# Performance work log

Measured on AMD Instinct MI355X. Metric: run time of the kernel, lower is better.

Reference implementation:

```python
import jax, jax.numpy as jnp
import numpy as np

N = 50000      # nodes per side
E = 800000     # edges per side
G = 1024       # graphs per batch
VOCAB = 100000
EMB, GH, EH, OUT = 128, 256, 256, 128
HID = GH + EH


def setup_inputs() -> dict:
    key = jax.random.key(0)
    ks = jax.random.split(key, 32)

    def xav(k, shape):
        lim = float(np.sqrt(6.0 / (shape[0] + shape[1])))
        return jax.random.uniform(k, shape, jnp.float32, -lim, lim)

    inp = {
        "x1": jax.random.randint(ks[0], (N,), 0, 11),
        "edge_index1": jax.random.randint(ks[1], (2, E), 0, N),
        "ent1": jax.random.randint(ks[2], (G,), 0, VOCAB),
        "batch1": jnp.sort(jax.random.randint(ks[3], (N,), 0, G)),
        "x2": jax.random.randint(ks[4], (N,), 0, 11),
        "edge_index2": jax.random.randint(ks[5], (2, E), 0, N),
        "ent2": jax.random.randint(ks[6], (G,), 0, VOCAB),
        "batch2": jnp.sort(jax.random.randint(ks[7], (N,), 0, G)),
        # shared GCN params (xavier weights, zero biases as in _reset_params)
        "atom_emb": xav(ks[8], (11, EMB)),
        "gW1": xav(ks[9], (EMB, GH)), "gb1": jnp.zeros((GH,), jnp.float32),
        "gW2": xav(ks[10], (GH, GH)), "gb2": jnp.zeros((GH,), jnp.float32),
        "fcW": xav(ks[11], (GH, GH)), "fcb": jnp.zeros((GH,), jnp.float32),
        # shared entity encoder params
        "ent_emb": xav(ks[12], (VOCAB, EMB)),
        "eW1": xav(ks[13], (EMB, EH)), "eb1": jnp.zeros((EH,), jnp.float32),
        "eW2": xav(ks[14], (EH, EH)), "eb2": jnp.zeros((EH,), jnp.float32),
        # decoder params
        "dW1": xav(ks[15], (HID, HID)), "db1": jnp.zeros((HID,), jnp.float32),
        "dW2": xav(ks[16], (HID, HID)), "db2": jnp.zeros((HID,), jnp.float32),
        "dW3": xav(ks[17], (HID, OUT)), "db3": jnp.zeros((OUT,), jnp.float32),
    }
    return inp


def _gcn_conv(x, W, b, src, dst, n):
    # PyG GCNConv: self-loops + symmetric normalization, out[dst] += norm * (x@W)[src]
    h = x @ W                                   # [n, d_out]
    loop = jnp.arange(n)
    s = jnp.concatenate([src, loop])
    d = jnp.concatenate([dst, loop])
    deg = jax.ops.segment_sum(jnp.ones_like(s, h.dtype), d, num_segments=n)
    dinv = jnp.where(deg > 0, jax.lax.rsqrt(jnp.maximum(deg, 1e-12)), 0.0)
    norm = dinv[s] * dinv[d]                    # [E+n]
    out = jax.ops.segment_sum(h[s] * norm[:, None], d, num_segments=n)
    return out + b


def _gcn_branch(x, edge_index, batch, atom_emb, gW1, gb1, gW2, gb2, fcW, fcb):
    src, dst = edge_index[0], edge_index[1]
    h = atom_emb[x]                             # [N, EMB]
    h = jax.nn.relu(_gcn_conv(h, gW1, gb1, src, dst, N))
    h = jax.nn.relu(_gcn_conv(h, gW2, gb2, src, dst, N))
    # global mean pool per graph
    counts = jax.ops.segment_sum(jnp.ones((N,), h.dtype), batch, num_segments=G)
    pooled = jax.ops.segment_sum(h, batch, num_segments=G) / jnp.maximum(counts, 1.0)[:, None]
    return pooled @ fcW + fcb                   # [G, GH]


def _enc(ent, ent_emb, eW1, eb1, eW2, eb2):
    e = jax.nn.relu(ent_emb[ent])
    e = jax.nn.relu(e @ eW1 + eb1)
    return jax.nn.relu(e @ eW2 + eb2)           # [G, EH]


def reference(x1, edge_index1, ent1, batch1, x2, edge_index2, ent2, batch2,
              atom_emb, gW1, gb1, gW2, gb2, fcW, fcb,
              ent_emb, eW1, eb1, eW2, eb2,
              dW1, db1, dW2, db2, dW3, db3):
    g1 = _gcn_branch(x1, edge_index1, batch1, atom_emb, gW1, gb1, gW2, gb2, fcW, fcb)
    g2 = _gcn_branch(x2, edge_index2, batch2, atom_emb, gW1, gb1, gW2, gb2, fcW, fcb)
    e1 = _enc(ent1, ent_emb, eW1, eb1, eW2, eb2)
    e2 = _enc(ent2, ent_emb, eW1, eb1, eW2, eb2)
    eg1 = jnp.concatenate([g1, e1], axis=1)     # [G, GH+EH]
    eg2 = jnp.concatenate([g2, e2], axis=1)
    egs = jax.nn.relu(eg1 + eg2)
    h = jax.nn.relu(egs @ dW1 + db1)
    h = jax.nn.relu(h @ dW2 + db2)
    return h @ dW3 + db3                        # [G, OUT]
```

## Files before the change

kernel.cpp:

```cpp
#include <hip/hip_runtime.h>
#include <hip/hip_fp16.h>

static constexpr int kN = 50000;
static constexpr int kE = 800000;
static constexpr int kG = 1024;
static constexpr int kEMB = 128;
static constexpr int kGH = 256;
static constexpr int kEH = 256;
static constexpr int kOUT = 128;
static constexpr int kHID = 512;
static constexpr int kNB = (kN + 255) / 256;
static constexpr int kMD = 64;
static constexpr int kNBKT = 196;
static constexpr int kEPB = 3125;
static constexpr int kPBLK = 256;

typedef __attribute__((ext_vector_type(8))) _Float16 half8v;
typedef __attribute__((ext_vector_type(4))) _Float16 half4v;
typedef __attribute__((ext_vector_type(4))) float floatx4;
typedef __attribute__((ext_vector_type(2))) float floatx2;


#define HS_SCALE 128.0f
#define HS_INV   (1.0f / 128.0f)

__device__ inline void acc_fp8x4(unsigned int w, float& a0, float& a1, float& a2, float& a3) {
    floatx2 lo = __builtin_amdgcn_cvt_pk_f32_fp8(w, false);
    floatx2 hi = __builtin_amdgcn_cvt_pk_f32_fp8(w, true);
    a0 += lo[0]; a1 += lo[1]; a2 += hi[0]; a3 += hi[1];
}

__device__ inline float grp16_reduce(float v) {
    int x;
    x = __builtin_amdgcn_update_dpp(0, __float_as_int(v), 0x121, 0xF, 0xF, true);
    v += __int_as_float(x);
    x = __builtin_amdgcn_update_dpp(0, __float_as_int(v), 0x122, 0xF, 0xF, true);
    v += __int_as_float(x);
    x = __builtin_amdgcn_update_dpp(0, __float_as_int(v), 0x124, 0xF, 0xF, true);
    v += __int_as_float(x);
    x = __builtin_amdgcn_update_dpp(0, __float_as_int(v), 0x128, 0xF, 0xF, true);
    v += __int_as_float(x);
    return v;
}

__global__ void prep_kernel(const float* __restrict__ atom_emb, const float* __restrict__ gW1,
                            const float* __restrict__ gW2,
                            float* __restrict__ M11, _Float16* __restrict__ w2t) {
    int i = blockIdx.x * 256 + threadIdx.x;
    if (blockIdx.x < 256) {
        int k = i >> 8, n = i & 255;
        w2t[(size_t)n * kGH + k] = (_Float16)gW2[(size_t)k * kGH + n];
    } else {
        int j = i - 65536;
        if (j < 11 * kGH) {
            int r = j >> 8, c = j & 255;
            float s = 0.f;
            for (int k = 0; k < kEMB; k++) s += atom_emb[r * kEMB + k] * gW1[k * kGH + c];
            M11[j] = s;
        }
    }
}

__global__ void wtrans_kernel(const float* __restrict__ dW1, const float* __restrict__ dW2,
                              const float* __restrict__ dW3, const float* __restrict__ fcW,
                              const float* __restrict__ eW1, const float* __restrict__ eW2,
                              _Float16* __restrict__ dW1t, _Float16* __restrict__ dW2t,
                              _Float16* __restrict__ dW3t, _Float16* __restrict__ fcWt,
                              _Float16* __restrict__ eW1t, _Float16* __restrict__ eW2t) {
    int b = blockIdx.x;
    const float* src; _Float16* dst; int K, N, j0;
    if (b < 1024)      { src = dW1; dst = dW1t; K = 512; N = 512; j0 = b * 256; }
    else if (b < 2048) { src = dW2; dst = dW2t; K = 512; N = 512; j0 = (b - 1024) * 256; }
    else if (b < 2304) { src = dW3; dst = dW3t; K = 512; N = 128; j0 = (b - 2048) * 256; }
    else if (b < 2560) { src = fcW; dst = fcWt; K = 256; N = 256; j0 = (b - 2304) * 256; }
    else if (b < 2688) { src = eW1; dst = eW1t; K = 128; N = 256; j0 = (b - 2560) * 256; }
    else               { src = eW2; dst = eW2t; K = 256; N = 256; j0 = (b - 2688) * 256; }
    int j = j0 + threadIdx.x;
    int n = j / K, k = j - n * K;
    dst[j] = (_Float16)src[(size_t)k * N + n];
}

__global__ void binp1_kernel(const int* __restrict__ ei1, const int* __restrict__ ei2,
                             int* __restrict__ poff) {
    int side = blockIdx.y;
    const int* dst = (side ? ei2 : ei1) + kE;
    __shared__ int hist[kNBKT];
    int t = threadIdx.x;
    if (t < kNBKT) hist[t] = 0;
    __syncthreads();
    int base = blockIdx.x * kEPB;
    for (int j = t; j < kEPB; j += 256)
        atomicAdd(&hist[dst[base + j] >> 8], 1);
    __syncthreads();
    if (t < kNBKT) poff[((side * kNBKT + t) << 8) | blockIdx.x] = hist[t];
}

__global__ void scanA_kernel(int* __restrict__ poff, int* __restrict__ btot) {
    int b = blockIdx.x, side = blockIdx.y, t = threadIdx.x;
    __shared__ int s[256];
    int idx = ((side * kNBKT + b) << 8) | t;
    int v = poff[idx];
    s[t] = v;
    __syncthreads();
    for (int o = 1; o < 256; o <<= 1) {
        int u = (t >= o) ? s[t - o] : 0;
        __syncthreads();
        s[t] += u;
        __syncthreads();
    }
    poff[idx] = s[t] - v;
    if (t == 255) btot[side * kNBKT + b] = s[255];
}

__global__ void scanB_kernel(const int* __restrict__ btot, int* __restrict__ bbase) {
    int side = blockIdx.x, t = threadIdx.x;
    __shared__ int s[256];
    int v = (t < kNBKT) ? btot[side * kNBKT + t] : 0;
    s[t] = v;
    __syncthreads();
    for (int o = 1; o < 256; o <<= 1) {
        int u = (t >= o) ? s[t - o] : 0;
        __syncthreads();
        s[t] += u;
        __syncthreads();
    }
    if (t < kNBKT) bbase[side * (kNBKT + 1) + t] = s[t] - v;
    if (t == 255) bbase[side * (kNBKT + 1) + kNBKT] = s[255];
}

__launch_bounds__(256)
__global__ void binp2_kernel(const int* __restrict__ ei1, const int* __restrict__ ei2,
                             const int* __restrict__ poff, const int* __restrict__ bbase,
                             unsigned int* __restrict__ ebuf) {
    int side = blockIdx.y, blk = blockIdx.x, t = threadIdx.x;
    const int* ei = side ? ei2 : ei1;
    __shared__ int hist[kNBKT], lb[kNBKT], gb[kNBKT], scanbuf[256];
    __shared__ unsigned int sorted[kEPB];
    if (t < kNBKT) hist[t] = 0;
    __syncthreads();
    int base = blk * kEPB;
    for (int j = t; j < kEPB; j += 256)
        atomicAdd(&hist[ei[kE + base + j] >> 8], 1);
    __syncthreads();
    int v = (t < kNBKT) ? hist[t] : 0;
    scanbuf[t] = v;
    __syncthreads();
    for (int o = 1; o < 256; o <<= 1) {
        int u = (t >= o) ? scanbuf[t - o] : 0;
        __syncthreads();
        scanbuf[t] += u;
        __syncthreads();
    }
    if (t < kNBKT) {
        lb[t] = scanbuf[t] - v;
        gb[t] = bbase[side * (kNBKT + 1) + t] + poff[((side * kNBKT + t) << 8) | blk];
        hist[t] = 0;
    }
    __syncthreads();
    for (int j = t; j < kEPB; j += 256) {
        int s_ = ei[base + j];
        int d  = ei[kE + base + j];
        int b  = d >> 8;
        int r  = atomicAdd(&hist[b], 1);
        sorted[lb[b] + r] = ((unsigned int)d << 16) | (unsigned int)s_;
    }
    __syncthreads();
    for (int j = t; j < kEPB; j += 256) {
        unsigned int val = sorted[j];
        int b = val >> 24;
        int gpos = gb[b] + (j - lb[b]);
        ebuf[(size_t)side * kE + gpos] = val;
    }
}

__global__ void binp3_kernel(const unsigned int* __restrict__ ebuf, const int* __restrict__ bbase,
                             unsigned short* __restrict__ col_ell, int* __restrict__ counts) {
    int b = blockIdx.x, side = blockIdx.y, t = threadIdx.x;
    __shared__ int cnt[256];
    cnt[t] = 0;
    __syncthreads();
    int start = bbase[side * (kNBKT + 1) + b];
    int end   = bbase[side * (kNBKT + 1) + b + 1];
    for (int k = start + t; k < end; k += 256) {
        unsigned int v = ebuf[(size_t)side * kE + k];
        int d8 = (v >> 16) & 255;
        int slot = atomicAdd(&cnt[d8], 1);
        if (slot > kMD - 1) slot = kMD - 1;
        int node = (b << 8) | d8;
        col_ell[((size_t)side * kN + node) * kMD + slot] = (unsigned short)(v & 0xFFFFu);
    }
    __syncthreads();
    int node = (b << 8) | t;
    if (node < kN) counts[side * kN + node] = cnt[t];
}

__global__ void dinvx_kernel(const int* __restrict__ counts, float* __restrict__ dinv,
                             int2* __restrict__ xd,
                             const int* __restrict__ x1, const int* __restrict__ x2) {
    int side = blockIdx.y;
    int i = blockIdx.x * 256 + threadIdx.x;
    if (i >= kN) return;
    int v = counts[side * kN + i];
    float dv = rsqrtf((float)(v + 1));
    dinv[side * kN + i] = dv;
    const int* x = side ? x2 : x1;
    xd[side * kN + i] = make_int2(x[i], __float_as_int(dv));
}

__global__ void conv1_combine_kernel(const int2* __restrict__ xd,
                                     const int* __restrict__ counts,
                                     const unsigned short* __restrict__ col_ell,
                                     const float* __restrict__ M11,
                                     const float* __restrict__ bias,
                                     _Float16* __restrict__ out) {
    int side = blockIdx.y;
    const int2* xdb = xd + (size_t)side * kN;
    const int* deg = counts + side * kN;
    const unsigned short* ci = col_ell + (size_t)side * kN * kMD;
    _Float16* ob = out + (size_t)side * kN * kGH;

    int tid = threadIdx.x;
    int sub = tid & 15;
    int v = blockIdx.x * 16 + (tid >> 4);

    int cnt = min(deg[v], kMD);
    const unsigned short* cv = ci + (size_t)v * kMD;
    float wt[11];
    #pragma unroll
    for (int t = 0; t < 11; t++) wt[t] = 0.f;
    for (int base = 0; base < cnt; base += 16) {
        int e = base + sub;
        int xs = 15; float ds = 0.f;
        if (e < cnt) {
            int2 t = xdb[(int)cv[e]];
            xs = t.x; ds = __int_as_float(t.y);
        }
        #pragma unroll
        for (int t = 0; t < 11; t++) wt[t] += (xs == t) ? ds : 0.f;
    }
    #pragma unroll
    for (int t = 0; t < 11; t++) wt[t] = grp16_reduce(wt[t]);

    int2 xv = xdb[v];
    float dv = __int_as_float(xv.y);
    #pragma unroll
    for (int q = 0; q < 4; q++) {
        int c = q * 64 + sub * 4;
        float4 bia = *(const float4*)(bias + c);
        float4 m = *(const float4*)(M11 + xv.x * kGH + c);
        float4 acc = make_float4(dv * m.x, dv * m.y, dv * m.z, dv * m.w);
        #pragma unroll
        for (int t = 0; t < 11; t++) {
            float w = wt[t];
            float4 mt = *(const float4*)(M11 + t * kGH + c);
            acc.x += w * mt.x; acc.y += w * mt.y;
            acc.z += w * mt.z; acc.w += w * mt.w;
        }
        half4v o;
        o[0] = (_Float16)fmaxf(dv * acc.x + bia.x, 0.f);
        o[1] = (_Float16)fmaxf(dv * acc.y + bia.y, 0.f);
        o[2] = (_Float16)fmaxf(dv * acc.z + bia.z, 0.f);
        o[3] = (_Float16)fmaxf(dv * acc.w + bia.w, 0.f);
        *(half4v*)(ob + (size_t)v * kGH + c) = o;
    }
}

__launch_bounds__(256)
__global__ void gemm2_mfma_kernel(const _Float16* __restrict__ A,
                                  const _Float16* __restrict__ Bt,
                                  const float* __restrict__ dinv,
                                  unsigned char* __restrict__ C) {
    __shared__ _Float16 As[128][72];
    __shared__ _Float16 Bs[128][72];

    int side = blockIdx.z;
    const _Float16* Ab = A + (size_t)side * kN * kGH;
    const float* db = dinv + (size_t)side * kN;
    unsigned char* Cb = C + (size_t)side * kN * kGH;

    int tid = threadIdx.x;
    int wave = tid >> 6, lane = tid & 63;
    int quad = lane >> 4, r = lane & 15;
    int wm = wave >> 1, wn = wave & 1;
    int row0 = blockIdx.x * 128;
    int col0 = blockIdx.y * 128;

    floatx4 acc[4][4];
    #pragma unroll
    for (int i = 0; i < 4; i++)
        #pragma unroll
        for (int j = 0; j < 4; j++) acc[i][j] = (floatx4){0.f, 0.f, 0.f, 0.f};

    for (int k0 = 0; k0 < kGH; k0 += 64) {
        #pragma unroll
        for (int u = 0; u < 4; u++) {
            int idx = tid + u * 256;
            int row = idx >> 3;
            int seg = (idx & 7) * 8;
            int gr = row0 + row;
            if (gr >= kN) gr = kN - 1;
            *(half8v*)&As[row][seg] = *(const half8v*)(Ab + (size_t)gr * kGH + k0 + seg);
            *(half8v*)&Bs[row][seg] = *(const half8v*)(Bt + (size_t)(col0 + row) * kGH + k0 + seg);
        }
        __syncthreads();
        #pragma unroll
        for (int ks = 0; ks < 2; ks++) {
            half8v af[4], bf[4];
            #pragma unroll
            for (int mt = 0; mt < 4; mt++)
                af[mt] = *(const half8v*)&As[wm * 64 + mt * 16 + r][ks * 32 + quad * 8];
            #pragma unroll
            for (int nt = 0; nt < 4; nt++)
                bf[nt] = *(const half8v*)&Bs[wn * 64 + nt * 16 + r][ks * 32 + quad * 8];
            #pragma unroll
            for (int mt = 0; mt < 4; mt++)
                #pragma unroll
                for (int nt = 0; nt < 4; nt++)
                    acc[mt][nt] = __builtin_amdgcn_mfma_f32_16x16x32_f16(af[mt], bf[nt],
                                                                         acc[mt][nt], 0, 0, 0);
        }
        __syncthreads();
    }

    #pragma unroll
    for (int mt = 0; mt < 4; mt++) {
        #pragma unroll
        for (int i = 0; i < 4; i++) {
            int grow = row0 + wm * 64 + mt * 16 + quad * 4 + i;
            if (grow >= kN) continue;
            float rsq = db[grow] * HS_SCALE;
            #pragma unroll
            for (int nt = 0; nt < 4; nt++) {
                int gcol = col0 + wn * 64 + nt * 16 + r;
                float q = acc[mt][nt][i] * rsq;
                Cb[(size_t)grow * kGH + gcol] =
                    (unsigned char)__builtin_amdgcn_cvt_pk_fp8_f32(q, q, 0, false);
            }
        }
    }
}

__launch_bounds__(256)
__global__ void gemm_tail_kernel(const _Float16* __restrict__ A,
                                 const _Float16* __restrict__ Bt,
                                 void* __restrict__ Cout,
                                 int N, int K,
                                 const float* __restrict__ bias,
                                 int relu, int f32out) {
    __shared__ _Float16 As[64][72];
    __shared__ _Float16 Bs[64][72];
    int tid = threadIdx.x;
    int wave = tid >> 6, lane = tid & 63;
    int quad = lane >> 4, r = lane & 15;
    int wm = wave >> 1, wn = wave & 1;
    int row0 = blockIdx.x * 64, col0 = blockIdx.y * 64;

    floatx4 acc[2][2];
    #pragma unroll
    for (int i = 0; i < 2; i++)
        #pragma unroll
        for (int j = 0; j < 2; j++) acc[i][j] = (floatx4){0.f, 0.f, 0.f, 0.f};

    for (int k0 = 0; k0 < K; k0 += 64) {
        #pragma unroll
        for (int u = 0; u < 2; u++) {
            int idx = tid + u * 256;
            int row = idx >> 3;
            int seg = (idx & 7) * 8;
            *(half8v*)&As[row][seg] = *(const half8v*)(A + (size_t)(row0 + row) * K + k0 + seg);
            *(half8v*)&Bs[row][seg] = *(const half8v*)(Bt + (size_t)(col0 + row) * K + k0 + seg);
        }
        __syncthreads();
        #pragma unroll
        for (int ks = 0; ks < 2; ks++) {
            half8v af[2], bf[2];
            #pragma unroll
            for (int mt = 0; mt < 2; mt++)
                af[mt] = *(const half8v*)&As[wm * 32 + mt * 16 + r][ks * 32 + quad * 8];
            #pragma unroll
            for (int nt = 0; nt < 2; nt++)
                bf[nt] = *(const half8v*)&Bs[wn * 32 + nt * 16 + r][ks * 32 + quad * 8];
            #pragma unroll
            for (int mt = 0; mt < 2; mt++)
                #pragma unroll
                for (int nt = 0; nt < 2; nt++)
                    acc[mt][nt] = __builtin_amdgcn_mfma_f32_16x16x32_f16(af[mt], bf[nt],
                                                                         acc[mt][nt], 0, 0, 0);
        }
        __syncthreads();
    }

    #pragma unroll
    for (int mt = 0; mt < 2; mt++) {
        #pragma unroll
        for (int i = 0; i < 4; i++) {
            int grow = row0 + wm * 32 + mt * 16 + quad * 4 + i;
            #pragma unroll
            for (int nt = 0; nt < 2; nt++) {
                int gcol = col0 + wn * 32 + nt * 16 + r;
                float v = acc[mt][nt][i] + bias[gcol];
                if (relu) v = fmaxf(v, 0.f);
                if (f32out) ((float*)Cout)[(size_t)grow * N + gcol] = v;
                else ((_Float16*)Cout)[(size_t)grow * N + gcol] = (_Float16)v;
            }
        }
    }
}

__global__ void aggregate2_kernel(const unsigned char* __restrict__ hs, const float* __restrict__ dinv,
                                  const int* __restrict__ counts,
                                  const unsigned short* __restrict__ col_ell,
                                  const float* __restrict__ bias, _Float16* __restrict__ out) {
    int side = blockIdx.y;
    const unsigned char* hb = hs + (size_t)side * kN * kGH;
    const float* dv_ = dinv + side * kN;
    const int* deg = counts + side * kN;
    const unsigned short* ci = col_ell + (size_t)side * kN * kMD;
    _Float16* ob = out + (size_t)side * kN * kGH;

    int wave = threadIdx.x >> 6;
    int lane = threadIdx.x & 63;
    int v = blockIdx.x * 4 + wave;
    if (v >= kN) return;
    int c = lane * 4;
    float4 bia = *(const float4*)(bias + c);
    float dv = dv_[v];
    float a0 = 0.f, a1 = 0.f, a2 = 0.f, a3 = 0.f;
    acc_fp8x4(*(const unsigned int*)(hb + (size_t)v * kGH + c), a0, a1, a2, a3);
    int cnt = min(deg[v], kMD);
    int idxl = (lane < cnt) ? (int)ci[(size_t)v * kMD + lane] : 0;
    int j = 0;
    for (; j + 16 <= cnt; j += 16) {
        unsigned int w[16];
        #pragma unroll
        for (int u = 0; u < 16; u++)
            w[u] = *(const unsigned int*)(hb + (size_t)__shfl(idxl, j + u) * kGH + c);
        #pragma unroll
        for (int u = 0; u < 16; u++) acc_fp8x4(w[u], a0, a1, a2, a3);
    }
    for (; j + 8 <= cnt; j += 8) {
        unsigned int w[8];
        #pragma unroll
        for (int u = 0; u < 8; u++)
            w[u] = *(const unsigned int*)(hb + (size_t)__shfl(idxl, j + u) * kGH + c);
        #pragma unroll
        for (int u = 0; u < 8; u++) acc_fp8x4(w[u], a0, a1, a2, a3);
    }
    for (; j < cnt; j++)
        acc_fp8x4(*(const unsigned int*)(hb + (size_t)__shfl(idxl, j) * kGH + c),
                  a0, a1, a2, a3);
    float f = dv * HS_INV;
    half4v o;
    o[0] = (_Float16)fmaxf(f * a0 + bia.x, 0.f);
    o[1] = (_Float16)fmaxf(f * a1 + bia.y, 0.f);
    o[2] = (_Float16)fmaxf(f * a2 + bia.z, 0.f);
    o[3] = (_Float16)fmaxf(f * a3 + bia.w, 0.f);
    __builtin_nontemporal_store(o, (half4v*)(ob + (size_t)v * kGH + c));
}

__global__ void pool_kernel(const _Float16* __restrict__ h,
                            const int* __restrict__ batch1, const int* __restrict__ batch2,
                            _Float16* __restrict__ pooled16) {
    int side = blockIdx.y;
    const _Float16* hb = h + (size_t)side * kN * kGH;
    const int* batch = side ? batch2 : batch1;
    int g = blockIdx.x;
    int lo = 0, hi = kN;
    while (lo < hi) { int mid = (lo + hi) >> 1; if (batch[mid] < g) lo = mid + 1; else hi = mid; }
    int start = lo;
    lo = start; hi = kN;
    while (lo < hi) { int mid = (lo + hi) >> 1; if (batch[mid] < g + 1) lo = mid + 1; else hi = mid; }
    int end = lo;
    int c = threadIdx.x;
    float s = 0.f;
    for (int v = start; v < end; v++) s += (float)hb[(size_t)v * kGH + c];
    pooled16[(size_t)(side * kG + g) * kGH + c] = (_Float16)(s / fmaxf((float)(end - start), 1.0f));
}

__global__ void egather_kernel(const float* __restrict__ emb,
                               const int* __restrict__ ent1, const int* __restrict__ ent2,
                               _Float16* __restrict__ e16) {
    int rr = blockIdx.x;
    int idx = (rr < kG) ? ent1[rr] : ent2[rr - kG];
    int k = threadIdx.x;
    e16[(size_t)rr * kEMB + k] = (_Float16)fmaxf(emb[(size_t)idx * kEMB + k], 0.f);
}

__global__ void egsprep_kernel(const _Float16* __restrict__ gfc16,
                               const _Float16* __restrict__ ento16,
                               _Float16* __restrict__ egs16) {
    int idx = blockIdx.x * 256 + threadIdx.x;
    int g = idx >> 6;
    int k8 = (idx & 63) * 8;
    const _Float16* src = (k8 < kGH) ? gfc16 : ento16;
    int kk = (k8 < kGH) ? k8 : k8 - kGH;
    half8v a = *(const half8v*)(src + (size_t)g * kGH + kk);
    half8v b = *(const half8v*)(src + (size_t)(g + kG) * kGH + kk);
    half8v o;
    #pragma unroll
    for (int u = 0; u < 8; u++) o[u] = (_Float16)fmaxf((float)a[u] + (float)b[u], 0.f);
    *(half8v*)(egs16 + (size_t)g * kHID + k8) = o;
}

static inline char* carve(char*& p, size_t bytes) {
    char* r = p;
    p += (bytes + 255) & ~(size_t)255;
    return r;
}

extern "C" void kernel_launch(void* const* d_in, const int* in_sizes, int n_in,
                              void* d_out, int out_size, void* d_ws, size_t ws_size,
                              hipStream_t stream) {
    const int*   x1       = (const int*)d_in[0];
    const int*   ei1      = (const int*)d_in[1];
    const int*   ent1     = (const int*)d_in[2];
    const int*   batch1   = (const int*)d_in[3];
    const int*   x2       = (const int*)d_in[4];
    const int*   ei2      = (const int*)d_in[5];
    const int*   ent2     = (const int*)d_in[6];
    const int*   batch2   = (const int*)d_in[7];
    const float* atom_emb = (const float*)d_in[8];
    const float* gW1      = (const float*)d_in[9];
    const float* gb1      = (const float*)d_in[10];
    const float* gW2      = (const float*)d_in[11];
    const float* gb2      = (const float*)d_in[12];
    const float* fcW      = (const float*)d_in[13];
    const float* fcb      = (const float*)d_in[14];
    const float* ent_emb  = (const float*)d_in[15];
    const float* eW1      = (const float*)d_in[16];
    const float* eb1      = (const float*)d_in[17];
    const float* eW2      = (const float*)d_in[18];
    const float* eb2      = (const float*)d_in[19];
    const float* dW1      = (const float*)d_in[20];
    const float* db1      = (const float*)d_in[21];
    const float* dW2      = (const float*)d_in[22];
    const float* db2      = (const float*)d_in[23];
    const float* dW3      = (const float*)d_in[24];
    const float* db3      = (const float*)d_in[25];
    float* out = (float*)d_out;

    char* p = (char*)d_ws;
    _Float16* h2_h   = (_Float16*)carve(p, (size_t)2 * kN * kGH * 2);
    unsigned char* hs8 = (unsigned char*)carve(p, (size_t)2 * kN * kGH);
    unsigned short* col_ell = (unsigned short*)carve(p, (size_t)2 * kN * kMD * 2);
    unsigned int* ebuf = (unsigned int*)carve(p, (size_t)2 * kE * 4);
    int*   poff    = (int*)  carve(p, (size_t)2 * kNBKT * 256 * 4);
    int*   btot    = (int*)  carve(p, (size_t)2 * kNBKT * 4);
    int*   bbase   = (int*)  carve(p, (size_t)2 * (kNBKT + 1) * 4);
    int*   counts  = (int*)  carve(p, (size_t)2 * kN * 4);
    float* dinv    = (float*)carve(p, (size_t)2 * kN * 4);
    int2*  xd      = (int2*) carve(p, (size_t)2 * kN * 8);
    float* M11     = (float*)carve(p, 11 * kGH * 4);
    _Float16* w2t  = (_Float16*)carve(p, (size_t)kGH * kGH * 2);
    _Float16* pooled16 = (_Float16*)carve(p, (size_t)2 * kG * kGH * 2);
    _Float16* gfc16    = (_Float16*)carve(p, (size_t)2 * kG * kGH * 2);
    _Float16* e16      = (_Float16*)carve(p, (size_t)2 * kG * kEMB * 2);
    _Float16* etmp16   = (_Float16*)carve(p, (size_t)2 * kG * kEH * 2);
    _Float16* ento16   = (_Float16*)carve(p, (size_t)2 * kG * kEH * 2);
    _Float16* egs16    = (_Float16*)carve(p, (size_t)kG * kHID * 2);
    _Float16* dh1_16   = (_Float16*)carve(p, (size_t)kG * kHID * 2);
    _Float16* dh2_16   = (_Float16*)carve(p, (size_t)kG * kHID * 2);
    _Float16* dW1t = (_Float16*)carve(p, (size_t)kHID * kHID * 2);
    _Float16* dW2t = (_Float16*)carve(p, (size_t)kHID * kHID * 2);
    _Float16* dW3t = (_Float16*)carve(p, (size_t)kOUT * kHID * 2);
    _Float16* fcWt = (_Float16*)carve(p, (size_t)kGH * kGH * 2);
    _Float16* eW1t = (_Float16*)carve(p, (size_t)kEH * kEMB * 2);
    _Float16* eW2t = (_Float16*)carve(p, (size_t)kEH * kEH * 2);

    prep_kernel<<<267, 256, 0, stream>>>(atom_emb, gW1, gW2, M11, w2t);
    wtrans_kernel<<<2944, 256, 0, stream>>>(dW1, dW2, dW3, fcW, eW1, eW2,
                                            dW1t, dW2t, dW3t, fcWt, eW1t, eW2t);
    binp1_kernel<<<dim3(kPBLK, 2), 256, 0, stream>>>(ei1, ei2, poff);
    scanA_kernel<<<dim3(kNBKT, 2), 256, 0, stream>>>(poff, btot);
    scanB_kernel<<<2, 256, 0, stream>>>(btot, bbase);
    binp2_kernel<<<dim3(kPBLK, 2), 256, 0, stream>>>(ei1, ei2, poff, bbase, ebuf);
    binp3_kernel<<<dim3(kNBKT, 2), 256, 0, stream>>>(ebuf, bbase, col_ell, counts);
    dinvx_kernel<<<dim3(kNB, 2), 256, 0, stream>>>(counts, dinv, xd, x1, x2);
    conv1_combine_kernel<<<dim3(kN / 16, 2), 256, 0, stream>>>(xd, counts, col_ell,
                                                               M11, gb1, h2_h);

    gemm2_mfma_kernel<<<dim3((kN + 127) / 128, kGH / 128, 2), 256, 0, stream>>>(h2_h, w2t,
                                                                                dinv, hs8);
    aggregate2_kernel<<<dim3((kN + 3) / 4, 2), 256, 0, stream>>>(hs8, dinv, counts, col_ell,
                                                                 gb2, h2_h);
    pool_kernel<<<dim3(kG, 2), 256, 0, stream>>>(h2_h, batch1, batch2, pooled16);
    egather_kernel<<<2 * kG, 128, 0, stream>>>(ent_emb, ent1, ent2, e16);

    gemm_tail_kernel<<<dim3(2 * kG / 64, kGH / 64), 256, 0, stream>>>(
        pooled16, fcWt, gfc16, kGH, kGH, fcb, 0, 0);
    gemm_tail_kernel<<<dim3(2 * kG / 64, kEH / 64), 256, 0, stream>>>(
        e16, eW1t, etmp16, kEH, kEMB, eb1, 1, 0);
    gemm_tail_kernel<<<dim3(2 * kG / 64, kEH / 64), 256, 0, stream>>>(
        etmp16, eW2t, ento16, kEH, kEH, eb2, 1, 0);
    egsprep_kernel<<<kG * kHID / 8 / 256, 256, 0, stream>>>(gfc16, ento16, egs16);
    gemm_tail_kernel<<<dim3(kG / 64, kHID / 64), 256, 0, stream>>>(
        egs16, dW1t, dh1_16, kHID, kHID, db1, 1, 0);
    gemm_tail_kernel<<<dim3(kG / 64, kHID / 64), 256, 0, stream>>>(
        dh1_16, dW2t, dh2_16, kHID, kHID, db2, 1, 0);
    gemm_tail_kernel<<<dim3(kG / 64, kOUT / 64), 256, 0, stream>>>(
        dh2_16, dW3t, out, kOUT, kHID, db3, 0, 1);
}
```

Baseline: 438.8 us.

## Fuse layer-2 aggregation with mean pooling and fold dinv into binning

The second-layer neighbour aggregation now runs per graph and accumulates the ReLU outputs straight into per-graph pooled sums in shared memory. This removes the write and re-read of the full fp16 node-feature matrix and one kernel launch. The degree-inverse and xd computation also moves into the binning kernel, which drops another launch. In exchange, parallelism falls to 2048 blocks of 4 waves, each handling about 49 nodes serially, so load balance and latency hiding may suffer.

```diff
diff --git a/kernel.cpp b/kernel.cpp
--- a/kernel.cpp
+++ b/kernel.cpp
@@ -174,7 +174,9 @@
 }
 
 __global__ void binp3_kernel(const unsigned int* __restrict__ ebuf, const int* __restrict__ bbase,
-                             unsigned short* __restrict__ col_ell, int* __restrict__ counts) {
+                             unsigned short* __restrict__ col_ell, int* __restrict__ counts,
+                             float* __restrict__ dinv, int2* __restrict__ xd,
+                             const int* __restrict__ x1, const int* __restrict__ x2) {
     int b = blockIdx.x, side = blockIdx.y, t = threadIdx.x;
     __shared__ int cnt[256];
     cnt[t] = 0;
@@ -191,20 +193,14 @@
     }
     __syncthreads();
     int node = (b << 8) | t;
-    if (node < kN) counts[side * kN + node] = cnt[t];
-}
-
-__global__ void dinvx_kernel(const int* __restrict__ counts, float* __restrict__ dinv,
-                             int2* __restrict__ xd,
-                             const int* __restrict__ x1, const int* __restrict__ x2) {
-    int side = blockIdx.y;
-    int i = blockIdx.x * 256 + threadIdx.x;
-    if (i >= kN) return;
-    int v = counts[side * kN + i];
-    float dv = rsqrtf((float)(v + 1));
-    dinv[side * kN + i] = dv;
-    const int* x = side ? x2 : x1;
-    xd[side * kN + i] = make_int2(x[i], __float_as_int(dv));
+    if (node < kN) {
+        int d = cnt[t];
+        counts[side * kN + node] = d;
+        float dv = rsqrtf((float)(d + 1));
+        dinv[side * kN + node] = dv;
+        const int* x = side ? x2 : x1;
+        xd[side * kN + node] = make_int2(x[node], __float_as_int(dv));
+    }
 }
 
 __global__ void conv1_combine_kernel(const int2* __restrict__ xd,
@@ -407,74 +403,75 @@
     }
 }
 
-__global__ void aggregate2_kernel(const unsigned char* __restrict__ hs, const float* __restrict__ dinv,
-                                  const int* __restrict__ counts,
-                                  const unsigned short* __restrict__ col_ell,
-                                  const float* __restrict__ bias, _Float16* __restrict__ out) {
+__global__ void aggpool_kernel(const unsigned char* __restrict__ hs, const float* __restrict__ dinv,
+                               const int* __restrict__ counts,
+                               const unsigned short* __restrict__ col_ell,
+                               const float* __restrict__ bias,
+                               const int* __restrict__ batch1, const int* __restrict__ batch2,
+                               _Float16* __restrict__ pooled16) {
     int side = blockIdx.y;
+    int g = blockIdx.x;
     const unsigned char* hb = hs + (size_t)side * kN * kGH;
     const float* dv_ = dinv + side * kN;
     const int* deg = counts + side * kN;
     const unsigned short* ci = col_ell + (size_t)side * kN * kMD;
-    _Float16* ob = out + (size_t)side * kN * kGH;
-
-    int wave = threadIdx.x >> 6;
-    int lane = threadIdx.x & 63;
-    int v = blockIdx.x * 4 + wave;
-    if (v >= kN) return;
-    int c = lane * 4;
-    float4 bia = *(const float4*)(bias + c);
-    float dv = dv_[v];
-    float a0 = 0.f, a1 = 0.f, a2 = 0.f, a3 = 0.f;
-    acc_fp8x4(*(const unsigned int*)(hb + (size_t)v * kGH + c), a0, a1, a2, a3);
-    int cnt = min(deg[v], kMD);
-    int idxl = (lane < cnt) ? (int)ci[(size_t)v * kMD + lane] : 0;
-    int j = 0;
-    for (; j + 16 <= cnt; j += 16) {
-        unsigned int w[16];
-        #pragma unroll
-        for (int u = 0; u < 16; u++)
-            w[u] = *(const unsigned int*)(hb + (size_t)__shfl(idxl, j + u) * kGH + c);
-        #pragma unroll
-        for (int u = 0; u < 16; u++) acc_fp8x4(w[u], a0, a1, a2, a3);
-    }
-    for (; j + 8 <= cnt; j += 8) {
-        unsigned int w[8];
-        #pragma unroll
-        for (int u = 0; u < 8; u++)
-            w[u] = *(const unsigned int*)(hb + (size_t)__shfl(idxl, j + u) * kGH + c);
-        #pragma unroll
-        for (int u = 0; u < 8; u++) acc_fp8x4(w[u], a0, a1, a2, a3);
-    }
-    for (; j < cnt; j++)
-        acc_fp8x4(*(const unsigned int*)(hb + (size_t)__shfl(idxl, j) * kGH + c),
-                  a0, a1, a2, a3);
-    float f = dv * HS_INV;
-    half4v o;
-    o[0] = (_Float16)fmaxf(f * a0 + bia.x, 0.f);
-    o[1] = (_Float16)fmaxf(f * a1 + bia.y, 0.f);
-    o[2] = (_Float16)fmaxf(f * a2 + bia.z, 0.f);
-    o[3] = (_Float16)fmaxf(f * a3 + bia.w, 0.f);
-    __builtin_nontemporal_store(o, (half4v*)(ob + (size_t)v * kGH + c));
-}
-
-__global__ void pool_kernel(const _Float16* __restrict__ h,
-                            const int* __restrict__ batch1, const int* __restrict__ batch2,
-                            _Float16* __restrict__ pooled16) {
-    int side = blockIdx.y;
-    const _Float16* hb = h + (size_t)side * kN * kGH;
     const int* batch = side ? batch2 : batch1;
-    int g = blockIdx.x;
+
     int lo = 0, hi = kN;
     while (lo < hi) { int mid = (lo + hi) >> 1; if (batch[mid] < g) lo = mid + 1; else hi = mid; }
     int start = lo;
     lo = start; hi = kN;
     while (lo < hi) { int mid = (lo + hi) >> 1; if (batch[mid] < g + 1) lo = mid + 1; else hi = mid; }
     int end = lo;
-    int c = threadIdx.x;
-    float s = 0.f;
-    for (int v = start; v < end; v++) s += (float)hb[(size_t)v * kGH + c];
-    pooled16[(size_t)(side * kG + g) * kGH + c] = (_Float16)(s / fmaxf((float)(end - start), 1.0f));
+
+    int wave = threadIdx.x >> 6;
+    int lane = threadIdx.x & 63;
+    int c = lane * 4;
+    float4 bia = *(const float4*)(bias + c);
+    float p0 = 0.f, p1 = 0.f, p2 = 0.f, p3 = 0.f;
+
+    for (int v = start + wave; v < end; v += 4) {
+        float dv = dv_[v];
+        float a0 = 0.f, a1 = 0.f, a2 = 0.f, a3 = 0.f;
+        acc_fp8x4(*(const unsigned int*)(hb + (size_t)v * kGH + c), a0, a1, a2, a3);
+        int cnt = min(deg[v], kMD);
+        int idxl = (lane < cnt) ? (int)ci[(size_t)v * kMD + lane] : 0;
+        int j = 0;
+        for (; j + 16 <= cnt; j += 16) {
+            unsigned int w[16];
+            #pragma unroll
+            for (int u = 0; u < 16; u++)
+                w[u] = *(const unsigned int*)(hb + (size_t)__shfl(idxl, j + u) * kGH + c);
+            #pragma unroll
+            for (int u = 0; u < 16; u++) acc_fp8x4(w[u], a0, a1, a2, a3);
+        }
+        for (; j + 8 <= cnt; j += 8) {
+            unsigned int w[8];
+            #pragma unroll
+            for (int u = 0; u < 8; u++)
+                w[u] = *(const unsigned int*)(hb + (size_t)__shfl(idxl, j + u) * kGH + c);
+            #pragma unroll
+            for (int u = 0; u < 8; u++) acc_fp8x4(w[u], a0, a1, a2, a3);
+        }
+        for (; j < cnt; j++)
+            acc_fp8x4(*(const unsigned int*)(hb + (size_t)__shfl(idxl, j) * kGH + c),
+                      a0, a1, a2, a3);
+        float f = dv * HS_INV;
+        p0 += fmaxf(f * a0 + bia.x, 0.f);
+        p1 += fmaxf(f * a1 + bia.y, 0.f);
+        p2 += fmaxf(f * a2 + bia.z, 0.f);
+        p3 += fmaxf(f * a3 + bia.w, 0.f);
+    }
+
+    __shared__ float psum[4][256];
+    *(float4*)&psum[wave][c] = make_float4(p0, p1, p2, p3);
+    __syncthreads();
+    int t = threadIdx.x;
+    if (t < 256) {
+        float s = psum[0][t] + psum[1][t] + psum[2][t] + psum[3][t];
+        float inv = 1.0f / fmaxf((float)(end - start), 1.0f);
+        pooled16[(size_t)(side * kG + g) * kGH + t] = (_Float16)(s * inv);
+    }
 }
 
 __global__ void egather_kernel(const float* __restrict__ emb,
@@ -574,16 +571,15 @@
     scanA_kernel<<<dim3(kNBKT, 2), 256, 0, stream>>>(poff, btot);
     scanB_kernel<<<2, 256, 0, stream>>>(btot, bbase);
     binp2_kernel<<<dim3(kPBLK, 2), 256, 0, stream>>>(ei1, ei2, poff, bbase, ebuf);
-    binp3_kernel<<<dim3(kNBKT, 2), 256, 0, stream>>>(ebuf, bbase, col_ell, counts);
-    dinvx_kernel<<<dim3(kNB, 2), 256, 0, stream>>>(counts, dinv, xd, x1, x2);
+    binp3_kernel<<<dim3(kNBKT, 2), 256, 0, stream>>>(ebuf, bbase, col_ell, counts,
+                                                     dinv, xd, x1, x2);
     conv1_combine_kernel<<<dim3(kN / 16, 2), 256, 0, stream>>>(xd, counts, col_ell,
                                                                M11, gb1, h2_h);
 
     gemm2_mfma_kernel<<<dim3((kN + 127) / 128, kGH / 128, 2), 256, 0, stream>>>(h2_h, w2t,
                                                                                 dinv, hs8);
-    aggregate2_kernel<<<dim3((kN + 3) / 4, 2), 256, 0, stream>>>(hs8, dinv, counts, col_ell,
-                                                                 gb2, h2_h);
-    pool_kernel<<<dim3(kG, 2), 256, 0, stream>>>(h2_h, batch1, batch2, pooled16);
+    aggpool_kernel<<<dim3(kG, 2), 256, 0, stream>>>(hs8, dinv, counts, col_ell,
+                                                    gb2, batch1, batch2, pooled16);
     egather_kernel<<<2 * kG, 128, 0, stream>>>(ent_emb, ent1, ent2, e16);
 
     gemm_tail_kernel<<<dim3(2 * kG / 64, kGH / 64), 256, 0, stream>>>(
```

Result: faster. 428.9 us (-2.3%).
